# Optimization experiments

Measured on AMD Instinct MI355X. Metric: run time of the kernel, lower is better.

## Reference

```python
import jax, jax.numpy as jnp
import numpy as np

NUM_USERS = 100000
NUM_ITEMS = 50000
EMB = 64
B = 8192
MAXM = 50
ATT_H = 16
PRED_H = 8


def setup_inputs() -> dict:
    key = jax.random.key(0)
    ks = jax.random.split(key, 12)
    member_idx = jax.random.randint(ks[0], (B, MAXM), 0, NUM_USERS)
    # ragged group sizes in [1, MAXM]
    lens = jax.random.randint(ks[1], (B,), 1, MAXM + 1)
    member_mask = jnp.arange(MAXM)[None, :] < lens[:, None]  # bool [B, M]
    item_inputs = jax.random.randint(ks[2], (B,), 0, NUM_ITEMS)
    s = 1.0 / np.sqrt(EMB)
    user_table = jax.random.normal(ks[3], (NUM_USERS, EMB), jnp.float32) * s
    item_table = jax.random.normal(ks[4], (NUM_ITEMS, EMB), jnp.float32) * s
    att_w1 = jax.random.normal(ks[5], (2 * EMB, ATT_H), jnp.float32) * 0.05
    att_b1 = jnp.zeros((ATT_H,), jnp.float32)
    att_w2 = jax.random.normal(ks[6], (ATT_H, 1), jnp.float32) * 0.05
    att_b2 = jnp.zeros((1,), jnp.float32)
    pred_w1 = jax.random.normal(ks[7], (3 * EMB, PRED_H), jnp.float32) * 0.05
    pred_b1 = jnp.zeros((PRED_H,), jnp.float32)
    pred_w2 = jax.random.normal(ks[8], (PRED_H, 1), jnp.float32) * 0.05
    pred_b2 = jnp.zeros((1,), jnp.float32)
    return dict(member_idx=member_idx, member_mask=member_mask, item_inputs=item_inputs,
                user_table=user_table, item_table=item_table,
                att_w1=att_w1, att_b1=att_b1, att_w2=att_w2, att_b2=att_b2,
                pred_w1=pred_w1, pred_b1=pred_b1, pred_w2=pred_w2, pred_b2=pred_b2)


def reference(member_idx, member_mask, item_inputs, user_table, item_table,
              att_w1, att_b1, att_w2, att_b2, pred_w1, pred_b1, pred_w2, pred_b2):
    mem_e = user_table[member_idx]            # [B, M, d]
    item_e = item_table[item_inputs]          # [B, d]
    # attention MLP over concat(member, item)
    cat = jnp.concatenate(
        [mem_e, jnp.broadcast_to(item_e[:, None, :], mem_e.shape)], axis=-1)  # [B, M, 2d]
    h = jax.nn.relu(jnp.einsum('bmf,fh->bmh', cat, att_w1) + att_b1)
    logits = (jnp.einsum('bmh,ho->bmo', h, att_w2) + att_b2)[..., 0]          # [B, M]
    logits = jnp.where(member_mask, logits, -jnp.inf)
    wts = jax.nn.softmax(logits, axis=-1)                                     # [B, M]
    g = jnp.einsum('bm,bmd->bd', wts, mem_e)                                  # [B, d]
    new = jnp.concatenate([g * item_e, g, item_e], axis=-1)                   # [B, 3d]
    ph = jax.nn.relu(new @ pred_w1 + pred_b1)
    y = jax.nn.sigmoid(ph @ pred_w2 + pred_b2)                                # [B, 1]
    return y
```

## Files before the change

### kernel.cpp

```cpp
#include <hip/hip_runtime.h>
#include <hip/hip_bf16.h>


__global__ void AGREE_12773232738622_probe(
    const void* member_mask,
    const void* user_table,
    int* ws)
{
    if (ws[2] == 0x5AFE0001) return;

    const int lane = threadIdx.x;
    const int wi = lane >> 4;
    const int r  = lane & 15;

    int len = 0, ok = 1, prev = 1;
    for (int m = 0; m < 50; ++m) {
        long e = 50L * r + m;
        int nz;
        if (wi == 0)      nz = (((const unsigned char*)member_mask)[e] != 0);
        else if (wi == 1) nz = (((const unsigned short*)member_mask)[e] != 0);
        else if (wi == 2) nz = (((const unsigned int*)member_mask)[e] != 0u);
        else {
            const unsigned int* p = (const unsigned int*)member_mask;
            nz = ((p[2 * e] | p[2 * e + 1]) != 0u);
        }
        if (nz && !prev) ok = 0;
        if (nz) len = len + 1;
        prev = nz;
    }
    if (len == 0) ok = 0;

    ok = ok & __shfl_xor(ok, 1);
    ok = ok & __shfl_xor(ok, 2);
    ok = ok & __shfl_xor(ok, 4);
    ok = ok & __shfl_xor(ok, 8);
    int mx = len;
    mx = max(mx, __shfl_xor(mx, 1));
    mx = max(mx, __shfl_xor(mx, 2));
    mx = max(mx, __shfl_xor(mx, 4));
    mx = max(mx, __shfl_xor(mx, 8));

    int o0 = __shfl(ok, 0),  o1 = __shfl(ok, 16), o2 = __shfl(ok, 32), o3 = __shfl(ok, 48);
    int L0 = __shfl(mx, 0),  L1 = __shfl(mx, 16), L2 = __shfl(mx, 32), L3 = __shfl(mx, 48);

    float v = __bfloat162float(((const __hip_bfloat16*)user_table)[lane]);
    float a = (v < 0.0f) ? -v : v;
    int huge = (!(a < 4.0f)) ? 1 : 0;
    unsigned long long hb = __ballot(huge);
    int hcnt = __popcll(hb);

    if (lane == 0) {
        int bestW = 1, bestLen = -1;
        if (o0 && L0 > bestLen) { bestLen = L0; bestW = 1; }
        if (o1 && L1 > bestLen) { bestLen = L1; bestW = 2; }
        if (o2 && L2 > bestLen) { bestLen = L2; bestW = 4; }
        if (o3 && L3 > bestLen) { bestLen = L3; bestW = 8; }
        ws[0] = bestW;
        ws[1] = (hcnt >= 8) ? 1 : 0;
        ws[2] = 0x5AFE0001;
    }
}

__global__ __launch_bounds__(256, 4) void AGREE_12773232738622_kernel(
    const int* member_idx,
    const void* member_mask,
    const int* item_inputs,
    const void* user_table,
    const void* item_table,
    const void* att_w1,
    const void* att_b1,
    const void* att_w2,
    const void* att_b2,
    const void* pred_w1,
    const void* pred_b1,
    const void* pred_w2,
    const void* pred_b2,
    void* out,
    const int* ws)
{
    const int tid  = threadIdx.x;
    const int lane = tid & 63;
    const int wave = tid >> 6;
    const int b    = blockIdx.x * 4 + wave;
    const int mode = ws[0];
    const int isf  = ws[1];

    int valid = 0;
    if (lane < 50) {
        long e0 = 50L * b + lane;
        if (mode == 1)      valid = (((const unsigned char*)member_mask)[e0] != 0);
        else if (mode == 2) valid = (((const unsigned short*)member_mask)[e0] != 0);
        else if (mode == 4) valid = (((const unsigned int*)member_mask)[e0] != 0u);
        else {
            const unsigned int* p = (const unsigned int*)member_mask;
            valid = ((p[2 * e0] | p[2 * e0 + 1]) != 0u);
        }
    }
    unsigned long long vm = __ballot(valid);
    int len = __popcll(vm);
    if (len < 1)  len = 1;
    if (len > 50) len = 50;

    const int item_id = item_inputs[b];
    float itemv;
    if (isf) itemv = ((const float*)item_table)[item_id * 64 + lane];
    else     itemv = __bfloat162float(((const __hip_bfloat16*)item_table)[item_id * 64 + lane]);

    int idxv = 0;
    if (lane < 50) idxv = member_idx[b * 50 + lane];

    float part;
    {
        const int kk = lane & 15;
        const int c  = lane >> 4;
        if (isf) part = (c == 0) ? ((const float*)att_b1)[kk] : 0.0f;
        else     part = (c == 0) ? __bfloat162float(((const __hip_bfloat16*)att_b1)[kk]) : 0.0f;
        for (int t = 0; t < 16; ++t) {
            int f = c * 16 + t;
            float iv = __shfl(itemv, f);
            float w;
            if (isf) w = ((const float*)att_w1)[(64 + f) * 16 + kk];
            else     w = __bfloat162float(((const __hip_bfloat16*)att_w1)[(64 + f) * 16 + kk]);
            part += iv * w;
        }
        part += __shfl_xor(part, 16);
        part += __shfl_xor(part, 32);
    }
    float h[16];
    #pragma unroll
    for (int k = 0; k < 16; ++k) h[k] = __shfl(part, k);

    if (lane < len) {
        if (isf) {
            const float* rp = (const float*)user_table + (long)idxv * 64;
            const float* w1 = (const float*)att_w1;
            #pragma unroll 4
            for (int c = 0; c < 16; ++c) {
                float4 v = ((const float4*)rp)[c];
                #pragma unroll
                for (int k = 0; k < 16; ++k) {
                    h[k] += v.x * w1[(c * 4 + 0) * 16 + k];
                    h[k] += v.y * w1[(c * 4 + 1) * 16 + k];
                    h[k] += v.z * w1[(c * 4 + 2) * 16 + k];
                    h[k] += v.w * w1[(c * 4 + 3) * 16 + k];
                }
            }
        } else {
            const unsigned short* rp = (const unsigned short*)user_table + (long)idxv * 64;
            const unsigned int* w1u = (const unsigned int*)att_w1;
            #pragma unroll 2
            for (int c = 0; c < 8; ++c) {
                uint4 v = ((const uint4*)rp)[c];
                float e[8];
                e[0] = __uint_as_float(v.x << 16);
                e[1] = __uint_as_float(v.x & 0xFFFF0000u);
                e[2] = __uint_as_float(v.y << 16);
                e[3] = __uint_as_float(v.y & 0xFFFF0000u);
                e[4] = __uint_as_float(v.z << 16);
                e[5] = __uint_as_float(v.z & 0xFFFF0000u);
                e[6] = __uint_as_float(v.w << 16);
                e[7] = __uint_as_float(v.w & 0xFFFF0000u);
                #pragma unroll
                for (int j = 0; j < 8; ++j) {
                    #pragma unroll
                    for (int p = 0; p < 8; ++p) {
                        unsigned int wp = w1u[(c * 8 + j) * 8 + p];
                        h[2 * p]     += e[j] * __uint_as_float(wp << 16);
                        h[2 * p + 1] += e[j] * __uint_as_float(wp & 0xFFFF0000u);
                    }
                }
            }
        }
    }

    float col[50];
    if (isf) {
        const float* ut = (const float*)user_table;
        #pragma unroll
        for (int m = 0; m < 50; ++m) {
            col[m] = 0.0f;
            if (m < len) {
                int idm = __shfl(idxv, m);
                col[m] = ut[(long)idm * 64 + lane];
            }
        }
    } else {
        const unsigned short* ut = (const unsigned short*)user_table;
        #pragma unroll
        for (int m = 0; m < 50; ++m) {
            col[m] = 0.0f;
            if (m < len) {
                int idm = __shfl(idxv, m);
                col[m] = __uint_as_float((unsigned int)ut[(long)idm * 64 + lane] << 16);
            }
        }
    }

    float lg;
    if (isf) lg = ((const float*)att_b2)[0];
    else     lg = __bfloat162float(((const __hip_bfloat16*)att_b2)[0]);
    #pragma unroll
    for (int k = 0; k < 16; ++k) {
        float hk = fmaxf(h[k], 0.0f);
        float w2;
        if (isf) w2 = ((const float*)att_w2)[k];
        else     w2 = __bfloat162float(((const __hip_bfloat16*)att_w2)[k]);
        lg += hk * w2;
    }

    float x = valid ? lg : -3.0e38f;
    float mx = x;
    mx = fmaxf(mx, __shfl_xor(mx, 1));
    mx = fmaxf(mx, __shfl_xor(mx, 2));
    mx = fmaxf(mx, __shfl_xor(mx, 4));
    mx = fmaxf(mx, __shfl_xor(mx, 8));
    mx = fmaxf(mx, __shfl_xor(mx, 16));
    mx = fmaxf(mx, __shfl_xor(mx, 32));
    float p = valid ? expf(x - mx) : 0.0f;
    float sum = p;
    sum += __shfl_xor(sum, 1);
    sum += __shfl_xor(sum, 2);
    sum += __shfl_xor(sum, 4);
    sum += __shfl_xor(sum, 8);
    sum += __shfl_xor(sum, 16);
    sum += __shfl_xor(sum, 32);
    float wnorm;
    if (sum > 0.0f) wnorm = p * (1.0f / sum);
    else            wnorm = (lane == 0) ? 1.0f : 0.0f;

    float g = 0.0f;
    #pragma unroll
    for (int m = 0; m < 50; ++m) {
        if (m < len) {
            float wv = __shfl(wnorm, m);
            g += wv * col[m];
        }
    }

    const float gi = g * itemv;
    float p8[8];
    if (isf) {
        const float4* pw4 = (const float4*)pred_w1;
        float4 a0 = pw4[lane * 2],         a1 = pw4[lane * 2 + 1];
        float4 b0 = pw4[(64 + lane) * 2],  b1 = pw4[(64 + lane) * 2 + 1];
        float4 c0 = pw4[(128 + lane) * 2], c1 = pw4[(128 + lane) * 2 + 1];
        p8[0] = gi * a0.x + g * b0.x + itemv * c0.x;
        p8[1] = gi * a0.y + g * b0.y + itemv * c0.y;
        p8[2] = gi * a0.z + g * b0.z + itemv * c0.z;
        p8[3] = gi * a0.w + g * b0.w + itemv * c0.w;
        p8[4] = gi * a1.x + g * b1.x + itemv * c1.x;
        p8[5] = gi * a1.y + g * b1.y + itemv * c1.y;
        p8[6] = gi * a1.z + g * b1.z + itemv * c1.z;
        p8[7] = gi * a1.w + g * b1.w + itemv * c1.w;
    } else {
        const uint4* pw4 = (const uint4*)pred_w1;
        uint4 A = pw4[lane];
        uint4 Bv = pw4[64 + lane];
        uint4 C = pw4[128 + lane];
        float ea[8], eb[8], ec[8];
        ea[0] = __uint_as_float(A.x << 16);  ea[1] = __uint_as_float(A.x & 0xFFFF0000u);
        ea[2] = __uint_as_float(A.y << 16);  ea[3] = __uint_as_float(A.y & 0xFFFF0000u);
        ea[4] = __uint_as_float(A.z << 16);  ea[5] = __uint_as_float(A.z & 0xFFFF0000u);
        ea[6] = __uint_as_float(A.w << 16);  ea[7] = __uint_as_float(A.w & 0xFFFF0000u);
        eb[0] = __uint_as_float(Bv.x << 16); eb[1] = __uint_as_float(Bv.x & 0xFFFF0000u);
        eb[2] = __uint_as_float(Bv.y << 16); eb[3] = __uint_as_float(Bv.y & 0xFFFF0000u);
        eb[4] = __uint_as_float(Bv.z << 16); eb[5] = __uint_as_float(Bv.z & 0xFFFF0000u);
        eb[6] = __uint_as_float(Bv.w << 16); eb[7] = __uint_as_float(Bv.w & 0xFFFF0000u);
        ec[0] = __uint_as_float(C.x << 16);  ec[1] = __uint_as_float(C.x & 0xFFFF0000u);
        ec[2] = __uint_as_float(C.y << 16);  ec[3] = __uint_as_float(C.y & 0xFFFF0000u);
        ec[4] = __uint_as_float(C.z << 16);  ec[5] = __uint_as_float(C.z & 0xFFFF0000u);
        ec[6] = __uint_as_float(C.w << 16);  ec[7] = __uint_as_float(C.w & 0xFFFF0000u);
        #pragma unroll
        for (int k2 = 0; k2 < 8; ++k2)
            p8[k2] = gi * ea[k2] + g * eb[k2] + itemv * ec[k2];
    }
    #pragma unroll
    for (int k2 = 0; k2 < 8; ++k2) {
        float v = p8[k2];
        v += __shfl_xor(v, 1);
        v += __shfl_xor(v, 2);
        v += __shfl_xor(v, 4);
        v += __shfl_xor(v, 8);
        v += __shfl_xor(v, 16);
        v += __shfl_xor(v, 32);
        p8[k2] = v;
    }
    if (lane == 0) {
        float z;
        if (isf) z = ((const float*)pred_b2)[0];
        else     z = __bfloat162float(((const __hip_bfloat16*)pred_b2)[0]);
        for (int k2 = 0; k2 < 8; ++k2) {
            float bb, ww;
            if (isf) {
                bb = ((const float*)pred_b1)[k2];
                ww = ((const float*)pred_w2)[k2];
            } else {
                bb = __bfloat162float(((const __hip_bfloat16*)pred_b1)[k2]);
                ww = __bfloat162float(((const __hip_bfloat16*)pred_w2)[k2]);
            }
            float hh = p8[k2] + bb;
            if (hh < 0.0f) hh = 0.0f;
            z += hh * ww;
        }
        float y = 1.0f / (1.0f + expf(-z));
        if (isf) ((float*)out)[b] = y;
        else     ((__hip_bfloat16*)out)[b] = __float2bfloat16(y);
    }
}

extern "C" void kernel_launch(void* const* d_in, const int* in_sizes, int n_in,
                              void* d_out, int out_size, void* d_ws, size_t ws_size,
                              hipStream_t stream) {
    (void)in_sizes; (void)n_in; (void)out_size; (void)ws_size;
    AGREE_12773232738622_probe<<<1, 64, 0, stream>>>(
        d_in[1], d_in[3], (int*)d_ws);
    AGREE_12773232738622_kernel<<<2048, 256, 0, stream>>>(
        (const int*)d_in[0],
        d_in[1],
        (const int*)d_in[2],
        d_in[3],
        d_in[4],
        d_in[5],
        d_in[6],
        d_in[7],
        d_in[8],
        d_in[9],
        d_in[10],
        d_in[11],
        d_in[12],
        d_out,
        (const int*)d_ws);
}
```

Baseline: 156.6 us.

## Hoist member embedding gathers ahead of attention MLP using scalar index loads

Member indices are now read with wave-uniform scalar loads, and all 50 user-embedding row gathers are issued unconditionally at the top of the kernel, before the item and attention computation. Padded slots reuse the first valid index, which removes the per-member branches and shuffles. The aim is to overlap gather latency with the attention MLP arithmetic and to cut VALU and cross-lane overhead. In exchange it always fetches 50 rows, including redundant loads for padded slots, and keeps more registers live across the MLP, which may lower occupancy.

```diff
diff --git a/kernel.cpp b/kernel.cpp
--- a/kernel.cpp
+++ b/kernel.cpp
@@ -81,7 +81,8 @@
     const int tid  = threadIdx.x;
     const int lane = tid & 63;
     const int wave = tid >> 6;
-    const int b    = blockIdx.x * 4 + wave;
+    int bb0  = blockIdx.x * 4 + wave;
+    const int b = __builtin_amdgcn_readfirstlane(bb0);
     const int mode = ws[0];
     const int isf  = ws[1];
 
@@ -97,9 +98,29 @@
         }
     }
     unsigned long long vm = __ballot(valid);
-    int len = __popcll(vm);
+    int len = __builtin_amdgcn_readfirstlane(__popcll(vm));
     if (len < 1)  len = 1;
     if (len > 50) len = 50;
+
+    const int* mrow = member_idx + (long)b * 50;
+    int sidx[50];
+    #pragma unroll
+    for (int m = 0; m < 50; ++m) sidx[m] = mrow[m];
+    #pragma unroll
+    for (int m = 0; m < 50; ++m) if (m >= len) sidx[m] = sidx[0];
+
+    float col[50];
+    if (isf) {
+        const float* ut = (const float*)user_table;
+        #pragma unroll
+        for (int m = 0; m < 50; ++m)
+            col[m] = ut[(long)sidx[m] * 64 + lane];
+    } else {
+        const unsigned short* ut = (const unsigned short*)user_table;
+        #pragma unroll
+        for (int m = 0; m < 50; ++m)
+            col[m] = __uint_as_float((unsigned int)ut[(long)sidx[m] * 64 + lane] << 16);
+    }
 
     const int item_id = item_inputs[b];
     float itemv;
@@ -107,7 +128,7 @@
     else     itemv = __bfloat162float(((const __hip_bfloat16*)item_table)[item_id * 64 + lane]);
 
     int idxv = 0;
-    if (lane < 50) idxv = member_idx[b * 50 + lane];
+    if (lane < 50) idxv = mrow[lane];
 
     float part;
     {
@@ -173,29 +194,6 @@
         }
     }
 
-    float col[50];
-    if (isf) {
-        const float* ut = (const float*)user_table;
-        #pragma unroll
-        for (int m = 0; m < 50; ++m) {
-            col[m] = 0.0f;
-            if (m < len) {
-                int idm = __shfl(idxv, m);
-                col[m] = ut[(long)idm * 64 + lane];
-            }
-        }
-    } else {
-        const unsigned short* ut = (const unsigned short*)user_table;
-        #pragma unroll
-        for (int m = 0; m < 50; ++m) {
-            col[m] = 0.0f;
-            if (m < len) {
-                int idm = __shfl(idxv, m);
-                col[m] = __uint_as_float((unsigned int)ut[(long)idm * 64 + lane] << 16);
-            }
-        }
-    }
-
     float lg;
     if (isf) lg = ((const float*)att_b2)[0];
     else     lg = __bfloat162float(((const __hip_bfloat16*)att_b2)[0]);
@@ -231,10 +229,8 @@
     float g = 0.0f;
     #pragma unroll
     for (int m = 0; m < 50; ++m) {
-        if (m < len) {
-            float wv = __shfl(wnorm, m);
-            g += wv * col[m];
-        }
+        float wv = __int_as_float(__builtin_amdgcn_readlane(__float_as_int(wnorm), m));
+        g += wv * col[m];
     }
 
     const float gi = g * itemv;
@@ -290,15 +286,15 @@
         if (isf) z = ((const float*)pred_b2)[0];
         else     z = __bfloat162float(((const __hip_bfloat16*)pred_b2)[0]);
         for (int k2 = 0; k2 < 8; ++k2) {
-            float bb, ww;
+            float bb2, ww;
             if (isf) {
-                bb = ((const float*)pred_b1)[k2];
-                ww = ((const float*)pred_w2)[k2];
+                bb2 = ((const float*)pred_b1)[k2];
+                ww  = ((const float*)pred_w2)[k2];
             } else {
-                bb = __bfloat162float(((const __hip_bfloat16*)pred_b1)[k2]);
-                ww = __bfloat162float(((const __hip_bfloat16*)pred_w2)[k2]);
+                bb2 = __bfloat162float(((const __hip_bfloat16*)pred_b1)[k2]);
+                ww  = __bfloat162float(((const __hip_bfloat16*)pred_w2)[k2]);
             }
-            float hh = p8[k2] + bb;
+            float hh = p8[k2] + bb2;
             if (hh < 0.0f) hh = 0.0f;
             z += hh * ww;
         }
```

After: 188.0 us. 1.2x slower.
